# Optimization experiments

Hardware: AMD Instinct MI355X
Metric: run time of the kernel (lower is better)

## Reference

```python
import jax, jax.numpy as jnp
import numpy as np

DIM = 768
NUM_HEADS = 12
POLY_DEG = 3
GRID = (24, 24)
BATCH = 16


def _make_powers():
    H, W = GRID
    ii, jj = np.meshgrid(np.arange(H), np.arange(W), indexing='ij')
    coords = np.stack([ii.ravel(), jj.ravel()], axis=-1).astype(np.float32)  # [HW, 2]
    dists = np.abs(coords[:, None, :] - coords[None, :, :]).sum(-1)  # L1 cdist [HW, HW]
    powers = np.stack([dists ** i for i in range(POLY_DEG + 1)], axis=0)  # [deg+1, HW, HW]
    return jnp.asarray(powers, dtype=jnp.float32)


def setup_inputs() -> dict:
    key = jax.random.key(0)
    ks = jax.random.split(key, 5)
    N = GRID[0] * GRID[1] + 1  # 577
    x = jax.random.normal(ks[0], (BATCH, N, DIM), dtype=jnp.float32)
    # nn.Linear weights stored as [in, out] for direct matmul; qkv_bias=False
    W_qkv = jax.random.normal(ks[1], (DIM, 3 * DIM), dtype=jnp.float32) * (DIM ** -0.5)
    W_proj = jax.random.normal(ks[2], (DIM, DIM), dtype=jnp.float32) * (DIM ** -0.5)
    b_proj = jnp.zeros((DIM,), dtype=jnp.float32)
    # small scale keeps polynomial bias (distances up to 46, cubed) numerically sane
    poly_coeffs = jax.random.normal(ks[3], (NUM_HEADS, POLY_DEG + 1), dtype=jnp.float32) * 0.01
    powers = _make_powers()
    return {"x": x, "W_qkv": W_qkv, "W_proj": W_proj, "b_proj": b_proj,
            "poly_coeffs": poly_coeffs, "powers": powers}


def reference(x, W_qkv, W_proj, b_proj, poly_coeffs, powers):
    B, N, C = x.shape
    h = NUM_HEADS
    d = C // h
    scale = d ** -0.5
    qkv = (x @ W_qkv).reshape(B, N, 3, h, d)
    qkv = jnp.transpose(qkv, (2, 0, 3, 1, 4))  # [3, B, h, N, d]
    q, k, v = qkv[0], qkv[1], qkv[2]
    # polynomial relative-position bias, padded with zeros for CLS row/col
    rpe = jnp.einsum('hd,dxy->hxy', poly_coeffs, powers)  # [h, HW, HW]
    rpe = jnp.pad(rpe, ((0, 0), (1, 0), (1, 0)))  # [h, N, N]
    attn = scale * jnp.einsum('bhnd,bhmd->bhnm', q, k) + rpe[None]
    attn = jax.nn.softmax(attn, axis=-1)
    out = jnp.einsum('bhnm,bhmd->bhnd', attn, v)
    out = jnp.transpose(out, (0, 2, 1, 3)).reshape(B, N, C)
    return out @ W_proj + b_proj
```

## Files before the change

kernel.cpp:

```cpp
#include <hip/hip_runtime.h>


using u16 = unsigned short;
using u32 = unsigned int;

typedef __bf16 bf16x8 __attribute__((ext_vector_type(8)));
typedef float f32x4 __attribute__((ext_vector_type(4)));

__device__ inline u16 f2bf(float f) {
    u32 u = __builtin_bit_cast(u32, f);
    u32 r = u + 0x7fffu + ((u >> 16) & 1u);
    return (u16)(r >> 16);
}
__device__ inline float bf2f(u16 x) {
    return __builtin_bit_cast(float, (u32)x << 16);
}

__device__ inline f32x4 mfma16(bf16x8 a, bf16x8 b, f32x4 c) {
    return __builtin_amdgcn_mfma_f32_16x16x32_bf16(a, b, c, 0, 0, 0);
}

__device__ inline float fexp2(float x) { return __builtin_amdgcn_exp2f(x); }

__device__ inline int xcd_remap(int bid, int nwg) {
    const int q = nwg >> 3, r = nwg & 7;
    const int xcd = bid & 7, idx = bid >> 3;
    return (xcd < r ? xcd * (q + 1) : r * (q + 1) + (xcd - r) * q) + idx;
}

__device__ inline float dpp_max16(float v) {
    int x;
    x = __builtin_amdgcn_update_dpp(0, __builtin_bit_cast(int, v), 0xB1, 0xF, 0xF, true);
    v = fmaxf(v, __builtin_bit_cast(float, x));
    x = __builtin_amdgcn_update_dpp(0, __builtin_bit_cast(int, v), 0x4E, 0xF, 0xF, true);
    v = fmaxf(v, __builtin_bit_cast(float, x));
    x = __builtin_amdgcn_update_dpp(0, __builtin_bit_cast(int, v), 0x124, 0xF, 0xF, true);
    v = fmaxf(v, __builtin_bit_cast(float, x));
    x = __builtin_amdgcn_update_dpp(0, __builtin_bit_cast(int, v), 0x128, 0xF, 0xF, true);
    v = fmaxf(v, __builtin_bit_cast(float, x));
    return v;
}
__device__ inline float dpp_sum16(float v) {
    int x;
    x = __builtin_amdgcn_update_dpp(0, __builtin_bit_cast(int, v), 0xB1, 0xF, 0xF, true);
    v += __builtin_bit_cast(float, x);
    x = __builtin_amdgcn_update_dpp(0, __builtin_bit_cast(int, v), 0x4E, 0xF, 0xF, true);
    v += __builtin_bit_cast(float, x);
    x = __builtin_amdgcn_update_dpp(0, __builtin_bit_cast(int, v), 0x124, 0xF, 0xF, true);
    v += __builtin_bit_cast(float, x);
    x = __builtin_amdgcn_update_dpp(0, __builtin_bit_cast(int, v), 0x128, 0xF, 0xF, true);
    v += __builtin_bit_cast(float, x);
    return v;
}

#define GLOAD_LDS16(g, l)                                                          \
    __builtin_amdgcn_global_load_lds((const __attribute__((address_space(1))) u32*)(g), \
                                     (__attribute__((address_space(3))) u32*)(l), 16, 0, 0)

#define BAR()    asm volatile("s_barrier" ::: "memory")
#define WAITV6() asm volatile("s_waitcnt vmcnt(6)" ::: "memory")
#define WAITV4() asm volatile("s_waitcnt vmcnt(4)" ::: "memory")
#define WAITV0() asm volatile("s_waitcnt vmcnt(0)" ::: "memory")

__global__ void k_prep(const float* __restrict__ x, const float* __restrict__ Wq,
                       const float* __restrict__ Wp, u16* __restrict__ xb,
                       u16* __restrict__ wqkv, u16* __restrict__ wprj) {
    const int tid0 = blockIdx.x * blockDim.x + threadIdx.x;
    const int stride = gridDim.x * blockDim.x;
    const int n4 = 9232 * 768 / 4;
    for (int i = tid0; i < n4; i += stride) {
        float4 v = ((const float4*)x)[i];
        ushort4 o;
        o.x = f2bf(v.x); o.y = f2bf(v.y); o.z = f2bf(v.z); o.w = f2bf(v.w);
        ((ushort4*)xb)[i] = o;
    }
    for (int i = tid0; i < 768 * 2304; i += stride) {
        int r = i / 2304, c = i - r * 2304;
        wqkv[(size_t)c * 768 + r] = f2bf(Wq[i]);
    }
    for (int i = tid0; i < 768 * 768; i += stride) {
        int r = i / 768, c = i - r * 768;
        wprj[(size_t)c * 768 + r] = f2bf(Wp[i]);
    }
}

template <int NJ>
__device__ inline void stageAB(const u16* __restrict__ Ag, const u16* __restrict__ Bg,
                               u16* L, int t) {
#pragma unroll
    for (int c = 0; c < 2; ++c) {
        const int p = c * 256 + t;
        const int row = p >> 2, ch = p & 3;
        GLOAD_LDS16(Ag + row * 768 + ((ch ^ ((row >> 1) & 3)) * 8), L + p * 8);
    }
#pragma unroll
    for (int c = 0; c < NJ / 2; ++c) {
        const int p = c * 256 + t;
        const int row = p >> 2, ch = p & 3;
        GLOAD_LDS16(Bg + row * 768 + ((ch ^ ((row >> 1) & 3)) * 8),
                    L + 4096 + p * 8);
    }
}
__device__ inline bf16x8 ldfrag32(const u16* base, int row, int slot) {
    return *(const bf16x8*)(base + row * 32 + ((slot ^ ((row >> 1) & 3)) * 8));
}

template <int MODE, int NB, int NJ>
__launch_bounds__(256, NJ == 8 ? 2 : 3)
__global__ void k_gemm(const u16* __restrict__ A, const u16* __restrict__ Bw,
                       u16* __restrict__ q_out, u16* __restrict__ k_out,
                       u16* __restrict__ v_out,
                       float* __restrict__ f_out, const float* __restrict__ bias) {
    constexpr int NT = 24;
    constexpr int M = 9232;
    constexpr int BN = NJ * 32;
    const int wgid = xcd_remap(blockIdx.x, gridDim.x);
    const int mbase = (wgid / NB) * 128;
    const int nbase = (wgid - (wgid / NB) * NB) * BN;
    __shared__ alignas(16) u16 lds[3][4096 + NJ * 1024];
    const int t = threadIdx.x;
    const int lane = t & 63, w = t >> 6;
    const int lr = lane & 15, lg = lane >> 4;
    const int wrow = (w >> 1) * 64, wcol = (w & 1) * (NJ * 16);
    const u16* Ag = A + (size_t)mbase * 768;
    const u16* Bg = Bw + (size_t)nbase * 768;
    f32x4 acc[4][NJ] = {};

    stageAB<NJ>(Ag, Bg, &lds[0][0], t);
    stageAB<NJ>(Ag + 32, Bg + 32, &lds[1][0], t);
    if (NJ == 8) { WAITV6(); } else { WAITV4(); }
    BAR();

    for (int kt = 0; kt < NT; ++kt) {
        const u16* Lc = &lds[kt % 3][0];
        const bool m2 = (kt + 2) < NT;
        if (m2)
            stageAB<NJ>(Ag + (kt + 2) * 32, Bg + (kt + 2) * 32,
                        &lds[(kt + 2) % 3][0], t);
        bf16x8 af[4], bv[NJ];
#pragma unroll
        for (int i = 0; i < 4; ++i)
            af[i] = ldfrag32(Lc, wrow + i * 16 + lr, lg);
#pragma unroll
        for (int j = 0; j < NJ; ++j)
            bv[j] = ldfrag32(Lc + 4096, wcol + j * 16 + lr, lg);
        __builtin_amdgcn_s_setprio(1);
#pragma unroll
        for (int i = 0; i < 4; ++i)
#pragma unroll
            for (int j = 0; j < NJ; ++j)
                acc[i][j] = mfma16(af[i], bv[j], acc[i][j]);
        __builtin_amdgcn_s_setprio(0);
        if (kt + 1 < NT) {
            if (m2) { if (NJ == 8) { WAITV6(); } else { WAITV4(); } }
            else    { WAITV0(); }
            BAR();
        }
    }

#pragma unroll
    for (int i = 0; i < 4; ++i) {
#pragma unroll
        for (int j = 0; j < NJ; ++j) {
            const int col = nbase + wcol + j * 16 + lr;
#pragma unroll
            for (int r = 0; r < 4; ++r) {
                const int row = mbase + wrow + i * 16 + 4 * lg + r;
                if (row < M) {
                    if (MODE == 0) {
                        const int bb = row / 577;
                        const int nn = row - bb * 577;
                        const int tt = col / 768;
                        const int rem = col - tt * 768;
                        const int hh = rem >> 6, dd = rem & 63;
                        const size_t bh = (size_t)bb * 12 + hh;
                        const u16 val = f2bf(acc[i][j][r]);
                        if (tt == 0)      q_out[(bh * 640 + nn) * 64 + dd] = val;
                        else if (tt == 1) k_out[(bh * 640 + nn) * 64 + dd] = val;
                        else              v_out[(bh * 64 + dd) * 640 + nn] = val;
                    } else {
                        f_out[(size_t)row * 768 + col] = acc[i][j][r] + bias[col];
                    }
                }
            }
        }
    }
}

__launch_bounds__(256, 3)
__global__ void k_attn(const u16* __restrict__ Qg, const u16* __restrict__ Kg,
                       const u16* __restrict__ Vtg, const float* __restrict__ coef,
                       u16* __restrict__ Og) {
    const int qt = blockIdx.x;
    const int bh = blockIdx.y;
    const int b = bh / 12, h = bh - b * 12;
    const int t = threadIdx.x;
    const int lane = t & 63, w = t >> 6;
    const int lr = lane & 15, lg = lane >> 4;
    __shared__ alignas(16) u16 Kl[2][4096];
    __shared__ alignas(16) u16 Vl[2][4096];
    __shared__ alignas(16) u16 Plds[4][16 * 72];
    __shared__ float lut[256];

    {
        const float l2e = 1.4426950408889634f;
        const float c0 = coef[h * 4 + 0] * l2e, c1 = coef[h * 4 + 1] * l2e,
                    c2 = coef[h * 4 + 2] * l2e, c3 = coef[h * 4 + 3] * l2e;
        const float d = (float)t;
        lut[t] = (t <= 46) ? (((c3 * d + c2) * d + c1) * d + c0) : 0.f;
    }

    const int qrow0 = qt * 64 + w * 16;
    const u16* qp = Qg + ((size_t)bh * 640 + qrow0 + lr) * 64;
    const bf16x8 qa0 = *(const bf16x8*)(qp + lg * 8);
    const bf16x8 qa1 = *(const bf16x8*)(qp + 32 + lg * 8);

    float gi[4], gj[4];
#pragma unroll
    for (int r = 0; r < 4; ++r) {
        const int n = qrow0 + 4 * lg + r;
        if (n == 0) { gi[r] = 100.f; gj[r] = 0.f; }
        else {
            const int nm1 = n - 1;
            const int qi = nm1 / 24;
            gi[r] = (float)qi;
            gj[r] = (float)(nm1 - qi * 24);
        }
    }

    float M[4], L[4];
#pragma unroll
    for (int r = 0; r < 4; ++r) { M[r] = -3e38f; L[r] = 0.f; }
    f32x4 acco[4] = {};
    const float scale2 = 0.125f * 1.4426950408889634f;
    const int ch0 = ((lg ^ (lr & 7))) * 8;

    const u16* Ksb = Kg + (size_t)bh * 640 * 64;
    const u16* Vsb = Vtg + (size_t)bh * 64 * 640;
    const int pr0 = t >> 3, pc0 = t & 7;
    const int pr1 = (256 + t) >> 3, pc1 = (256 + t) & 7;
    const int kd0 = pr0 * 64 + ((pc0 ^ (pr0 & 7)) * 8);
    const int kd1 = pr1 * 64 + ((pc1 ^ (pr1 & 7)) * 8);

    {
        uint4 k0 = *(const uint4*)(Ksb + pr0 * 64 + pc0 * 8);
        uint4 k1 = *(const uint4*)(Ksb + pr1 * 64 + pc1 * 8);
        uint4 v0 = *(const uint4*)(Vsb + (size_t)pr0 * 640 + pc0 * 8);
        uint4 v1 = *(const uint4*)(Vsb + (size_t)pr1 * 640 + pc1 * 8);
        *(uint4*)(&Kl[0][kd0]) = k0;
        *(uint4*)(&Kl[0][kd1]) = k1;
        *(uint4*)(&Vl[0][kd0]) = v0;
        *(uint4*)(&Vl[0][kd1]) = v1;
    }
    __syncthreads();
    int cur = 0;

    for (int kt = 0; kt < 10; ++kt) {
        const bool full = (kt < 9);
        uint4 nk0, nk1, nv0, nv1;
        if (full) {
            const u16* Ks = Ksb + (size_t)(kt + 1) * 64 * 64;
            const u16* Vs = Vsb + (size_t)(kt + 1) * 64;
            nk0 = *(const uint4*)(Ks + pr0 * 64 + pc0 * 8);
            nk1 = *(const uint4*)(Ks + pr1 * 64 + pc1 * 8);
            nv0 = *(const uint4*)(Vs + (size_t)pr0 * 640 + pc0 * 8);
            nv1 = *(const uint4*)(Vs + (size_t)pr1 * 640 + pc1 * 8);
        }
        const u16* Kc = &Kl[cur][0];
        const u16* Vc = &Vl[cur][0];

        f32x4 sac[4];
#pragma unroll
        for (int cb = 0; cb < 4; ++cb) {
            if (full || cb == 0) {
                const int row = cb * 16 + lr;
                const bf16x8 kb0 = *(const bf16x8*)(Kc + row * 64 + ch0);
                const bf16x8 kb1 = *(const bf16x8*)(Kc + row * 64 + (ch0 ^ 32));
                f32x4 z = {};
                z = mfma16(qa0, kb0, z);
                sac[cb] = mfma16(qa1, kb1, z);
            }
        }

        float s[4][4], tm[4];
#pragma unroll
        for (int r = 0; r < 4; ++r) tm[r] = -3e38f;
#pragma unroll
        for (int cb = 0; cb < 4; ++cb) {
            if (full || cb == 0) {
                const int m = kt * 64 + cb * 16 + lr;
                float ci, cj;
                if (m == 0) { ci = 200.f; cj = 0.f; }
                else {
                    const int mm1 = m - 1;
                    const int pi = mm1 / 24;
                    ci = (float)pi;
                    cj = (float)(mm1 - pi * 24);
                }
#pragma unroll
                for (int r = 0; r < 4; ++r) {
                    const float df = fabsf(gi[r] - ci) + fabsf(gj[r] - cj);
                    const int idx = (int)df;
                    float v = fmaf(sac[cb][r], scale2, lut[idx]);
                    if (!full) v = (lr == 0) ? v : -1e30f;
                    s[cb][r] = v;
                    tm[r] = fmaxf(tm[r], v);
                }
            } else {
#pragma unroll
                for (int r = 0; r < 4; ++r) s[cb][r] = -1e30f;
            }
        }
#pragma unroll
        for (int r = 0; r < 4; ++r) tm[r] = dpp_max16(tm[r]);

        float over = tm[0] - M[0];
        over = fmaxf(over, tm[1] - M[1]);
        over = fmaxf(over, tm[2] - M[2]);
        over = fmaxf(over, tm[3] - M[3]);
        if (__any(over > 11.5f)) {
#pragma unroll
            for (int r = 0; r < 4; ++r) {
                const float Mn = fmaxf(M[r], tm[r]);
                const float a = fexp2(M[r] - Mn);
                L[r] *= a;
                acco[0][r] *= a; acco[1][r] *= a;
                acco[2][r] *= a; acco[3][r] *= a;
                M[r] = Mn;
            }
        }

        u16* pw = &Plds[w][0];
#pragma unroll
        for (int cb = 0; cb < 4; ++cb)
#pragma unroll
            for (int r = 0; r < 4; ++r) {
                const float p = fexp2(s[cb][r] - M[r]);
                L[r] += p;
                pw[(4 * lg + r) * 72 + cb * 16 + lr] = f2bf(p);
            }
        const bf16x8 pa0 = *(const bf16x8*)(pw + lr * 72 + lg * 8);
        const bf16x8 pa1 = *(const bf16x8*)(pw + lr * 72 + 32 + lg * 8);
#pragma unroll
        for (int f = 0; f < 4; ++f) {
            const int vrow = f * 16 + lr;
            const bf16x8 vb0 = *(const bf16x8*)(Vc + vrow * 64 + ch0);
            acco[f] = mfma16(pa0, vb0, acco[f]);
            if (full) {
                const bf16x8 vb1 = *(const bf16x8*)(Vc + vrow * 64 + (ch0 ^ 32));
                acco[f] = mfma16(pa1, vb1, acco[f]);
            }
        }

        if (full) {
            __syncthreads();
            *(uint4*)(&Kl[cur ^ 1][kd0]) = nk0;
            *(uint4*)(&Kl[cur ^ 1][kd1]) = nk1;
            *(uint4*)(&Vl[cur ^ 1][kd0]) = nv0;
            *(uint4*)(&Vl[cur ^ 1][kd1]) = nv1;
            __syncthreads();
            cur ^= 1;
        }
    }

    float inv[4];
#pragma unroll
    for (int r = 0; r < 4; ++r) inv[r] = __builtin_amdgcn_rcpf(dpp_sum16(L[r]));
#pragma unroll
    for (int f = 0; f < 4; ++f)
#pragma unroll
        for (int r = 0; r < 4; ++r) {
            const int n = qrow0 + 4 * lg + r;
            Og[((size_t)b * 577 + n) * 768 + h * 64 + f * 16 + lr] =
                f2bf(acco[f][r] * inv[r]);
        }
}

__launch_bounds__(256)
__global__ void k_attn_last(const u16* __restrict__ Qg, const u16* __restrict__ Kg,
                            const u16* __restrict__ Vtg, const float* __restrict__ coef,
                            u16* __restrict__ Og) {
    const int bh = blockIdx.x;
    const int b = bh / 12, h = bh - b * 12;
    const int t = threadIdx.x;
    const int lane = t & 63, w = t >> 6;
    __shared__ float qs[64];
    __shared__ float ps[640];
    __shared__ float red[4];
    __shared__ float opart[4][64];
    const float l2e = 1.4426950408889634f;
    const float c0 = coef[h * 4 + 0] * l2e, c1 = coef[h * 4 + 1] * l2e,
                c2 = coef[h * 4 + 2] * l2e, c3 = coef[h * 4 + 3] * l2e;
    const float scale2 = 0.125f * l2e;

    if (t < 64) qs[t] = bf2f(Qg[((size_t)bh * 640 + 576) * 64 + t]);
    __syncthreads();

    float sv[3];
#pragma unroll
    for (int u = 0; u < 3; ++u) {
        const int k = t + u * 256;
        float s = -3e38f;
        if (k < 577) {
            const u16* kp = Kg + ((size_t)bh * 640 + k) * 64;
            float acc = 0.f;
            for (int j = 0; j < 64; ++j) acc += qs[j] * bf2f(kp[j]);
            float rv = 0.f;
            if (k >= 1) {
                const int km1 = k - 1;
                const int ki = km1 / 24;
                const float d = fabsf(23.f - (float)ki) + fabsf(23.f - (float)(km1 - ki * 24));
                rv = ((c3 * d + c2) * d + c1) * d + c0;
            }
            s = fmaf(acc, scale2, rv);
        }
        sv[u] = s;
    }
    float v = fmaxf(fmaxf(sv[0], sv[1]), sv[2]);
    v = fmaxf(v, __shfl_xor(v, 1));  v = fmaxf(v, __shfl_xor(v, 2));
    v = fmaxf(v, __shfl_xor(v, 4));  v = fmaxf(v, __shfl_xor(v, 8));
    v = fmaxf(v, __shfl_xor(v, 16)); v = fmaxf(v, __shfl_xor(v, 32));
    if (lane == 0) red[w] = v;
    __syncthreads();
    const float Mx = fmaxf(fmaxf(red[0], red[1]), fmaxf(red[2], red[3]));

    float lsum = 0.f;
#pragma unroll
    for (int u = 0; u < 3; ++u) {
        const int k = t + u * 256;
        const float p = (k < 577) ? fexp2(sv[u] - Mx) : 0.f;
        if (k < 640) ps[k] = p;
        lsum += p;
    }
    lsum += __shfl_xor(lsum, 1);  lsum += __shfl_xor(lsum, 2);
    lsum += __shfl_xor(lsum, 4);  lsum += __shfl_xor(lsum, 8);
    lsum += __shfl_xor(lsum, 16); lsum += __shfl_xor(lsum, 32);
    __syncthreads();
    if (lane == 0) red[w] = lsum;
    __syncthreads();
    const float Lx = red[0] + red[1] + red[2] + red[3];

    const int d = t & 63, qd = t >> 6;
    const u16* vp = Vtg + ((size_t)bh * 64 + d) * 640;
    float o = 0.f;
    for (int k = qd * 160; k < qd * 160 + 160; ++k) o += ps[k] * bf2f(vp[k]);
    opart[qd][d] = o;
    __syncthreads();
    if (t < 64) {
        const float oo = (opart[0][t] + opart[1][t] + opart[2][t] + opart[3][t]) / Lx;
        Og[((size_t)b * 577 + 576) * 768 + h * 64 + t] = f2bf(oo);
    }
}

extern "C" void kernel_launch(void* const* d_in, const int* in_sizes, int n_in,
                              void* d_out, int out_size, void* d_ws, size_t ws_size,
                              hipStream_t stream) {
    const float* x      = (const float*)d_in[0];
    const float* W_qkv  = (const float*)d_in[1];
    const float* W_proj = (const float*)d_in[2];
    const float* b_proj = (const float*)d_in[3];
    const float* coef   = (const float*)d_in[4];
    float* out = (float*)d_out;
    char* ws = (char*)d_ws;

    u16* xb   = (u16*)(ws + 0);
    u16* Og   = (u16*)(ws + 0);
    u16* wqkv = (u16*)(ws + 14180352);
    u16* wprj = (u16*)(ws + 17719296);
    u16* Qg   = (u16*)(ws + 18898944);
    u16* Kg   = (u16*)(ws + 34627584);
    u16* Vtg  = (u16*)(ws + 50356224);

    k_prep<<<2048, 256, 0, stream>>>(x, W_qkv, W_proj, xb, wqkv, wprj);

    k_gemm<0, 9, 8><<<9 * 73, 256, 0, stream>>>(xb, wqkv, Qg, Kg, Vtg,
                                                nullptr, nullptr);
    k_attn<<<dim3(9, 192), 256, 0, stream>>>(Qg, Kg, Vtg, coef, Og);
    k_attn_last<<<192, 256, 0, stream>>>(Qg, Kg, Vtg, coef, Og);
    k_gemm<1, 6, 4><<<6 * 73, 256, 0, stream>>>(Og, wprj, nullptr, nullptr,
                                                nullptr, out, b_proj);
}
```

Baseline: 184.5 us.

## Use square 128x128 GEMM tiles with 4-stage pipeline; peel last attention tile

The GEMM kernel drops its templated N-width and uses a fixed 128x128 tile with four LDS stages and three loads in flight. The QKV GEMM now launches 18 column blocks instead of 9, and the projection GEMM moves from a 128x128 to a 128x128 tile as well (from NJ=4, i.e. same width). In the attention kernel the partial last key tile is peeled out of the main loop, which removes per-iteration 'full' branches and one of the two barriers per iteration. The deeper pipeline uses more LDS, which may limit occupancy, and relies on the single barrier being enough for the double-buffered K/V writes.

```diff
diff --git a/kernel.cpp b/kernel.cpp
--- a/kernel.cpp
+++ b/kernel.cpp
@@ -58,7 +58,7 @@
                                      (__attribute__((address_space(3))) u32*)(l), 16, 0, 0)
 
 #define BAR()    asm volatile("s_barrier" ::: "memory")
-#define WAITV6() asm volatile("s_waitcnt vmcnt(6)" ::: "memory")
+#define WAITV8() asm volatile("s_waitcnt vmcnt(8)" ::: "memory")
 #define WAITV4() asm volatile("s_waitcnt vmcnt(4)" ::: "memory")
 #define WAITV0() asm volatile("s_waitcnt vmcnt(0)" ::: "memory")
 
@@ -84,76 +84,69 @@
     }
 }
 
-template <int NJ>
 __device__ inline void stageAB(const u16* __restrict__ Ag, const u16* __restrict__ Bg,
                                u16* L, int t) {
 #pragma unroll
     for (int c = 0; c < 2; ++c) {
         const int p = c * 256 + t;
         const int row = p >> 2, ch = p & 3;
-        GLOAD_LDS16(Ag + row * 768 + ((ch ^ ((row >> 1) & 3)) * 8), L + p * 8);
-    }
-#pragma unroll
-    for (int c = 0; c < NJ / 2; ++c) {
-        const int p = c * 256 + t;
-        const int row = p >> 2, ch = p & 3;
-        GLOAD_LDS16(Bg + row * 768 + ((ch ^ ((row >> 1) & 3)) * 8),
-                    L + 4096 + p * 8);
+        const int src = row * 768 + ((ch ^ ((row >> 1) & 3)) * 8);
+        GLOAD_LDS16(Ag + src, L + p * 8);
+        GLOAD_LDS16(Bg + src, L + 4096 + p * 8);
     }
 }
 __device__ inline bf16x8 ldfrag32(const u16* base, int row, int slot) {
     return *(const bf16x8*)(base + row * 32 + ((slot ^ ((row >> 1) & 3)) * 8));
 }
 
-template <int MODE, int NB, int NJ>
-__launch_bounds__(256, NJ == 8 ? 2 : 3)
+template <int MODE, int NB>
+__launch_bounds__(256, 2)
 __global__ void k_gemm(const u16* __restrict__ A, const u16* __restrict__ Bw,
                        u16* __restrict__ q_out, u16* __restrict__ k_out,
                        u16* __restrict__ v_out,
                        float* __restrict__ f_out, const float* __restrict__ bias) {
     constexpr int NT = 24;
     constexpr int M = 9232;
-    constexpr int BN = NJ * 32;
     const int wgid = xcd_remap(blockIdx.x, gridDim.x);
     const int mbase = (wgid / NB) * 128;
-    const int nbase = (wgid - (wgid / NB) * NB) * BN;
-    __shared__ alignas(16) u16 lds[3][4096 + NJ * 1024];
+    const int nbase = (wgid - (wgid / NB) * NB) * 128;
+    __shared__ alignas(16) u16 lds[4][8192];
     const int t = threadIdx.x;
     const int lane = t & 63, w = t >> 6;
     const int lr = lane & 15, lg = lane >> 4;
-    const int wrow = (w >> 1) * 64, wcol = (w & 1) * (NJ * 16);
+    const int wrow = (w >> 1) * 64, wcol = (w & 1) * 64;
     const u16* Ag = A + (size_t)mbase * 768;
     const u16* Bg = Bw + (size_t)nbase * 768;
-    f32x4 acc[4][NJ] = {};
-
-    stageAB<NJ>(Ag, Bg, &lds[0][0], t);
-    stageAB<NJ>(Ag + 32, Bg + 32, &lds[1][0], t);
-    if (NJ == 8) { WAITV6(); } else { WAITV4(); }
+    f32x4 acc[4][4] = {};
+
+    stageAB(Ag, Bg, &lds[0][0], t);
+    stageAB(Ag + 32, Bg + 32, &lds[1][0], t);
+    stageAB(Ag + 64, Bg + 64, &lds[2][0], t);
+    WAITV8();
     BAR();
 
     for (int kt = 0; kt < NT; ++kt) {
-        const u16* Lc = &lds[kt % 3][0];
-        const bool m2 = (kt + 2) < NT;
-        if (m2)
-            stageAB<NJ>(Ag + (kt + 2) * 32, Bg + (kt + 2) * 32,
-                        &lds[(kt + 2) % 3][0], t);
-        bf16x8 af[4], bv[NJ];
+        const u16* Lc = &lds[kt & 3][0];
+        if (kt + 3 < NT)
+            stageAB(Ag + (kt + 3) * 32, Bg + (kt + 3) * 32, &lds[(kt + 3) & 3][0], t);
+        bf16x8 af[4], bv[4];
 #pragma unroll
         for (int i = 0; i < 4; ++i)
             af[i] = ldfrag32(Lc, wrow + i * 16 + lr, lg);
 #pragma unroll
-        for (int j = 0; j < NJ; ++j)
+        for (int j = 0; j < 4; ++j)
             bv[j] = ldfrag32(Lc + 4096, wcol + j * 16 + lr, lg);
         __builtin_amdgcn_s_setprio(1);
 #pragma unroll
         for (int i = 0; i < 4; ++i)
 #pragma unroll
-            for (int j = 0; j < NJ; ++j)
+            for (int j = 0; j < 4; ++j)
                 acc[i][j] = mfma16(af[i], bv[j], acc[i][j]);
         __builtin_amdgcn_s_setprio(0);
         if (kt + 1 < NT) {
-            if (m2) { if (NJ == 8) { WAITV6(); } else { WAITV4(); } }
-            else    { WAITV0(); }
+            if (kt < NT - 3)       { WAITV8(); }
+            else if (kt == NT - 3) { WAITV4(); }
+            else                   { WAITV0(); }
             BAR();
         }
     }
@@ -161,7 +154,7 @@
 #pragma unroll
     for (int i = 0; i < 4; ++i) {
 #pragma unroll
-        for (int j = 0; j < NJ; ++j) {
+        for (int j = 0; j < 4; ++j) {
             const int col = nbase + wcol + j * 16 + lr;
 #pragma unroll
             for (int r = 0; r < 4; ++r) {
@@ -255,31 +248,26 @@
     __syncthreads();
     int cur = 0;
 
-    for (int kt = 0; kt < 10; ++kt) {
-        const bool full = (kt < 9);
-        uint4 nk0, nk1, nv0, nv1;
-        if (full) {
-            const u16* Ks = Ksb + (size_t)(kt + 1) * 64 * 64;
-            const u16* Vs = Vsb + (size_t)(kt + 1) * 64;
-            nk0 = *(const uint4*)(Ks + pr0 * 64 + pc0 * 8);
-            nk1 = *(const uint4*)(Ks + pr1 * 64 + pc1 * 8);
-            nv0 = *(const uint4*)(Vs + (size_t)pr0 * 640 + pc0 * 8);
-            nv1 = *(const uint4*)(Vs + (size_t)pr1 * 640 + pc1 * 8);
-        }
+    for (int kt = 0; kt < 9; ++kt) {
+        const u16* Ks = Ksb + (size_t)(kt + 1) * 64 * 64;
+        const u16* Vs = Vsb + (size_t)(kt + 1) * 64;
+        const uint4 nk0 = *(const uint4*)(Ks + pr0 * 64 + pc0 * 8);
+        const uint4 nk1 = *(const uint4*)(Ks + pr1 * 64 + pc1 * 8);
+        const uint4 nv0 = *(const uint4*)(Vs + (size_t)pr0 * 640 + pc0 * 8);
+        const uint4 nv1 = *(const uint4*)(Vs + (size_t)pr1 * 640 + pc1 * 8);
+
         const u16* Kc = &Kl[cur][0];
         const u16* Vc = &Vl[cur][0];
 
         f32x4 sac[4];
 #pragma unroll
         for (int cb = 0; cb < 4; ++cb) {
-            if (full || cb == 0) {
-                const int row = cb * 16 + lr;
-                const bf16x8 kb0 = *(const bf16x8*)(Kc + row * 64 + ch0);
-                const bf16x8 kb1 = *(const bf16x8*)(Kc + row * 64 + (ch0 ^ 32));
-                f32x4 z = {};
-                z = mfma16(qa0, kb0, z);
-                sac[cb] = mfma16(qa1, kb1, z);
-            }
+            const int row = cb * 16 + lr;
+            const bf16x8 kb0 = *(const bf16x8*)(Kc + row * 64 + ch0);
+            const bf16x8 kb1 = *(const bf16x8*)(Kc + row * 64 + (ch0 ^ 32));
+            f32x4 z = {};
+            z = mfma16(qa0, kb0, z);
+            sac[cb] = mfma16(qa1, kb1, z);
         }
 
         float s[4][4], tm[4];
@@ -287,28 +275,22 @@
         for (int r = 0; r < 4; ++r) tm[r] = -3e38f;
 #pragma unroll
         for (int cb = 0; cb < 4; ++cb) {
-            if (full || cb == 0) {
-                const int m = kt * 64 + cb * 16 + lr;
-                float ci, cj;
-                if (m == 0) { ci = 200.f; cj = 0.f; }
-                else {
-                    const int mm1 = m - 1;
-                    const int pi = mm1 / 24;
-                    ci = (float)pi;
-                    cj = (float)(mm1 - pi * 24);
-                }
-#pragma unroll
-                for (int r = 0; r < 4; ++r) {
-                    const float df = fabsf(gi[r] - ci) + fabsf(gj[r] - cj);
-                    const int idx = (int)df;
-                    float v = fmaf(sac[cb][r], scale2, lut[idx]);
-                    if (!full) v = (lr == 0) ? v : -1e30f;
-                    s[cb][r] = v;
-                    tm[r] = fmaxf(tm[r], v);
-                }
-            } else {
-#pragma unroll
-                for (int r = 0; r < 4; ++r) s[cb][r] = -1e30f;
+            const int m = kt * 64 + cb * 16 + lr;
+            float ci, cj;
+            if (m == 0) { ci = 200.f; cj = 0.f; }
+            else {
+                const int mm1 = m - 1;
+                const int pi = mm1 / 24;
+                ci = (float)pi;
+                cj = (float)(mm1 - pi * 24);
+            }
+#pragma unroll
+            for (int r = 0; r < 4; ++r) {
+                const float df = fabsf(gi[r] - ci) + fabsf(gj[r] - cj);
+                const int idx = (int)df;
+                const float v = fmaf(sac[cb][r], scale2, lut[idx]);
+                s[cb][r] = v;
+                tm[r] = fmaxf(tm[r], v);
             }
         }
 #pragma unroll
@@ -345,21 +327,67 @@
         for (int f = 0; f < 4; ++f) {
             const int vrow = f * 16 + lr;
             const bf16x8 vb0 = *(const bf16x8*)(Vc + vrow * 64 + ch0);
+            const bf16x8 vb1 = *(const bf16x8*)(Vc + vrow * 64 + (ch0 ^ 32));
             acco[f] = mfma16(pa0, vb0, acco[f]);
-            if (full) {
-                const bf16x8 vb1 = *(const bf16x8*)(Vc + vrow * 64 + (ch0 ^ 32));
-                acco[f] = mfma16(pa1, vb1, acco[f]);
-            }
-        }
-
-        if (full) {
-            __syncthreads();
-            *(uint4*)(&Kl[cur ^ 1][kd0]) = nk0;
-            *(uint4*)(&Kl[cur ^ 1][kd1]) = nk1;
-            *(uint4*)(&Vl[cur ^ 1][kd0]) = nv0;
-            *(uint4*)(&Vl[cur ^ 1][kd1]) = nv1;
-            __syncthreads();
-            cur ^= 1;
+            acco[f] = mfma16(pa1, vb1, acco[f]);
+        }
+
+        *(uint4*)(&Kl[cur ^ 1][kd0]) = nk0;
+        *(uint4*)(&Kl[cur ^ 1][kd1]) = nk1;
+        *(uint4*)(&Vl[cur ^ 1][kd0]) = nv0;
+        *(uint4*)(&Vl[cur ^ 1][kd1]) = nv1;
+        __syncthreads();
+        cur ^= 1;
+    }
+
+    {
+        const u16* Kc = &Kl[cur][0];
+        const u16* Vc = &Vl[cur][0];
+        const bf16x8 kb0 = *(const bf16x8*)(Kc + lr * 64 + ch0);
+        const bf16x8 kb1 = *(const bf16x8*)(Kc + lr * 64 + (ch0 ^ 32));
+        f32x4 z = {};
+        z = mfma16(qa0, kb0, z);
+        const f32x4 sac0 = mfma16(qa1, kb1, z);
+
+        float s0[4], tm[4];
+#pragma unroll
+        for (int r = 0; r < 4; ++r) {
+            const float df = fabsf(gi[r] - 23.f) + fabsf(gj[r] - 23.f);
+            float v = fmaf(sac0[r], scale2, lut[(int)df]);
+            v = (lr == 0) ? v : -1e30f;
+            s0[r] = v;
+            tm[r] = dpp_max16(v);
+        }
+        float over = tm[0] - M[0];
+        over = fmaxf(over, tm[1] - M[1]);
+        over = fmaxf(over, tm[2] - M[2]);
+        over = fmaxf(over, tm[3] - M[3]);
+        if (__any(over > 11.5f)) {
+#pragma unroll
+            for (int r = 0; r < 4; ++r) {
+                const float Mn = fmaxf(M[r], tm[r]);
+                const float a = fexp2(M[r] - Mn);
+                L[r] *= a;
+                acco[0][r] *= a; acco[1][r] *= a;
+                acco[2][r] *= a; acco[3][r] *= a;
+                M[r] = Mn;
+            }
+        }
+        u16* pw = &Plds[w][0];
+#pragma unroll
+        for (int cb = 0; cb < 4; ++cb)
+#pragma unroll
+            for (int r = 0; r < 4; ++r) {
+                const float p = (cb == 0) ? fexp2(s0[r] - M[r]) : 0.f;
+                L[r] += p;
+                pw[(4 * lg + r) * 72 + cb * 16 + lr] = f2bf(p);
+            }
+        const bf16x8 pa0 = *(const bf16x8*)(pw + lr * 72 + lg * 8);
+#pragma unroll
+        for (int f = 0; f < 4; ++f) {
+            const int vrow = f * 16 + lr;
+            const bf16x8 vb0 = *(const bf16x8*)(Vc + vrow * 64 + ch0);
+            acco[f] = mfma16(pa0, vb0, acco[f]);
         }
     }
 
@@ -473,10 +501,10 @@
 
     k_prep<<<2048, 256, 0, stream>>>(x, W_qkv, W_proj, xb, wqkv, wprj);
 
-    k_gemm<0, 9, 8><<<9 * 73, 256, 0, stream>>>(xb, wqkv, Qg, Kg, Vtg,
-                                                nullptr, nullptr);
+    k_gemm<0, 18><<<18 * 73, 256, 0, stream>>>(xb, wqkv, Qg, Kg, Vtg,
+                                               nullptr, nullptr);
     k_attn<<<dim3(9, 192), 256, 0, stream>>>(Qg, Kg, Vtg, coef, Og);
     k_attn_last<<<192, 256, 0, stream>>>(Qg, Kg, Vtg, coef, Og);
-    k_gemm<1, 6, 4><<<6 * 73, 256, 0, stream>>>(Og, wprj, nullptr, nullptr,
-                                                nullptr, out, b_proj);
-}
+    k_gemm<1, 6><<<6 * 73, 256, 0, stream>>>(Og, wprj, nullptr, nullptr,
+                                             nullptr, out, b_proj);
+}
```

Result: no change. 183.7 us (-0.4%).
